# Performance work log

Measured on AMD Instinct MI355X. Metric: run time of the kernel, lower is better.

The kernel has to match this reference:

```python
import jax, jax.numpy as jnp
import numpy as np

EPS = 1e-8

def mlp(x, w1, b1, w2, b2):
    return jnp.tanh(x @ w1 + b1) @ w2 + b2

def setup_inputs() -> dict:
    key = jax.random.key(0)
    ks = jax.random.split(key, 24)
    N_NEWS, N_USERS, N_ATR = 50000, 100000, 1000
    E_ATR, E_USR = 100000, 2000000
    D = 768
    def lin(k, fi, fo):
        return jax.random.normal(k, (fi, fo), jnp.float32) * (1.0 / np.sqrt(fi))
    inp = {
        'news_x': jax.random.normal(ks[0], (N_NEWS, D), jnp.float32),
        'users_x': jax.random.normal(ks[1], (N_USERS, 128), jnp.float32),
        'w1a': lin(ks[2], D, 256), 'b1a': jnp.zeros((256,), jnp.float32),
        'w1b': lin(ks[3], 256, 128), 'b1b': jnp.zeros((128,), jnp.float32),
        'wna': lin(ks[4], D + 128, 512), 'bna': jnp.zeros((512,), jnp.float32),
        'wnb': lin(ks[5], 512, 128), 'bnb': jnp.zeros((128,), jnp.float32),
        'wua': lin(ks[6], 256, 256), 'bua': jnp.zeros((256,), jnp.float32),
        'wub': lin(ks[7], 256, 128), 'bub': jnp.zeros((128,), jnp.float32),
        'atr_row': jax.random.randint(ks[8], (E_ATR,), 0, N_NEWS, jnp.int32),
        'atr_col': jax.random.randint(ks[9], (E_ATR,), 0, N_ATR, jnp.int32),
        'usr_row': jax.random.randint(ks[10], (E_USR,), 0, N_NEWS, jnp.int32),
        'usr_col': jax.random.randint(ks[11], (E_USR,), 0, N_USERS, jnp.int32),
        'n_news': N_NEWS, 'n_users': N_USERS, 'n_atr': N_ATR,
    }
    return inp

def reference(news_x, users_x, w1a, b1a, w1b, b1b, wna, bna, wnb, bnb,
              wua, bua, wub, bub, atr_row, atr_col, usr_row, usr_col,
              n_news, n_users, n_atr):
    dt = news_x.dtype
    ones_a = jnp.ones(atr_row.shape[0], dt)
    ones_u = jnp.ones(usr_row.shape[0], dt)
    # FirstConv: news -> attribute nodes (edge_index.t() @ news)
    deg_atr = jax.ops.segment_sum(ones_a, atr_col, num_segments=n_atr)
    agr_atr = jax.ops.segment_sum(news_x[atr_row], atr_col, num_segments=n_atr)
    agr_atr = agr_atr / (deg_atr[:, None] + EPS)
    atr_feats = mlp(agr_atr, w1a, b1a, w1b, b1b)  # [n_atr, 128]
    # NewsConv: attribute -> news (edge_index @ atr_feats), concat with news_x
    deg_news = jax.ops.segment_sum(ones_a, atr_row, num_segments=n_news)
    agr_news = jax.ops.segment_sum(atr_feats[atr_col], atr_row, num_segments=n_news)
    agr_news = agr_news / (deg_news[:, None] + EPS)
    news_out = mlp(jnp.concatenate([news_x, agr_news], axis=1), wna, bna, wnb, bnb)  # [n_news,128]
    # UserConv: news -> users (edge_index['users'].t() @ news), concat with users_x
    deg_usr = jax.ops.segment_sum(ones_u, usr_col, num_segments=n_users)
    agr_usr = jax.ops.segment_sum(news_out[usr_row], usr_col, num_segments=n_users)
    agr_usr = agr_usr / (deg_usr[:, None] + EPS)
    users_out = mlp(jnp.concatenate([users_x, agr_usr], axis=1), wua, bua, wub, bub)  # [n_users,128]
    # stack final news + user embeddings into one array
    return jnp.concatenate([news_out, users_out], axis=0)  # [n_news+n_users, 128]
```

## Files before the change

kernel.cpp:

```cpp
#include <hip/hip_runtime.h>

#define N_NEWS 50000
#define N_USERS 100000
#define N_ATR 1000
#define E_ATR 100000
#define E_USR 2000000
#define EPSF 1e-8f

#define ACAP 192
#define NCAP 24
#define P_USR 250
#define UPP 400
#define ACAPP 9216
#define EBLK_A 4096

typedef short s16x8 __attribute__((ext_vector_type(8)));
typedef float f32x4 __attribute__((ext_vector_type(4)));

__device__ inline ushort f2bf(float f) {
    uint u = __float_as_uint(f);
    u += 0x7fffu + ((u >> 16) & 1u);
    return (ushort)(u >> 16);
}
__device__ inline float bflo(uint v) { return __uint_as_float(v << 16); }
__device__ inline float bfhi(uint v) { return __uint_as_float(v & 0xffff0000u); }
__device__ inline float fast_tanh(float x) {
    x = fminf(fmaxf(x, -15.0f), 15.0f);
    float e = __expf(2.0f * x);
    return (e - 1.0f) / (e + 1.0f);
}

struct TrJob { const float* src; ushort* dst; int R, C, blkEnd; };

struct PrepArgs {
    const int *atr_row, *atr_col, *usr_row, *usr_col;
    int *cnt_atr, *cnt_news, *arena_cnt;
    int *ids_atr, *ids_news;
    unsigned long long* arena;
    const float *news_x, *users_x;
    ushort *news_bf, *users_bf;
    int pa, fa, tr, n1, n2;
    TrJob j[6];
};

__global__ void prep_k(PrepArgs A) {
    __shared__ float tile[32][33];
    __shared__ int cloc[256], cscn[256], sexc[256], cbase[256];
    __shared__ ushort stageI[EBLK_A];
    int b = blockIdx.x;
    int t = threadIdx.x;
    if (b < A.pa) {
        cloc[t] = 0;
        __syncthreads();
        int base = b * EBLK_A;
        int endE = base + EBLK_A; if (endE > E_USR) endE = E_USR;
        int n = endE - base;
        for (int e = base + t; e < endE; e += 256)
            atomicAdd(&cloc[A.usr_col[e] / UPP], 1);
        __syncthreads();
        cscn[t] = cloc[t];
        __syncthreads();
        for (int off = 1; off < 256; off <<= 1) {
            int v = (t >= off) ? cscn[t - off] : 0;
            __syncthreads();
            cscn[t] += v;
            __syncthreads();
        }
        sexc[t] = cscn[t] - cloc[t];
        if (t < P_USR) cbase[t] = atomicAdd(&A.arena_cnt[t], cloc[t]);
        cloc[t] = 0;
        __syncthreads();
        for (int e = base + t; e < endE; e += 256) {
            int p = A.usr_col[e] / UPP;
            int off = atomicAdd(&cloc[p], 1);
            stageI[sexc[p] + off] = (ushort)(e - base);
        }
        __syncthreads();
        for (int i = t; i < n; i += 256) {
            int e = base + stageI[i];
            int c = A.usr_col[e];
            int r = A.usr_row[e];
            int p = c / UPP;
            int dst = cbase[p] + (i - sexc[p]);
            if (dst < ACAPP)
                A.arena[(size_t)p * ACAPP + dst] =
                    ((unsigned long long)(uint)c << 32) | (uint)r;
        }
        return;
    }
    b -= A.pa;
    if (b < A.fa) {
        int total = 2 * E_ATR;
        int per = (total + A.fa - 1) / A.fa;
        int base = b * per;
        int endE = base + per; if (endE > total) endE = total;
        for (int e = base + t; e < endE; e += 256) {
            if (e < E_ATR) {
                int c = A.atr_col[e];
                int slot = atomicAdd(&A.cnt_atr[c], 1);
                if (slot < ACAP) A.ids_atr[(size_t)c * ACAP + slot] = A.atr_row[e];
            } else {
                int e2 = e - E_ATR;
                int r = A.atr_row[e2];
                int slot = atomicAdd(&A.cnt_news[r], 1);
                if (slot < NCAP) A.ids_news[(size_t)r * NCAP + slot] = A.atr_col[e2];
            }
        }
        return;
    }
    b -= A.fa;
    if (b < A.tr) {
        int ji = 0;
        while (b >= A.j[ji].blkEnd) ++ji;
        const TrJob& J = A.j[ji];
        int lb = b - (ji ? A.j[ji - 1].blkEnd : 0);
        int ctiles = J.C / 32;
        int bc = (lb % ctiles) * 32, br = (lb / ctiles) * 32;
        int tx = t & 31, ty = t >> 5;
        for (int i = 0; i < 4; ++i)
            tile[ty + i * 8][tx] = J.src[(size_t)(br + ty + i * 8) * J.C + bc + tx];
        __syncthreads();
        for (int i = 0; i < 4; ++i)
            J.dst[(size_t)(bc + ty + i * 8) * J.R + br + tx] = f2bf(tile[tx][ty + i * 8]);
        return;
    }
    b -= A.tr;
    int i = b * 256 + t;
    const float* src; ushort* dst;
    if (i < A.n1) { src = A.news_x; dst = A.news_bf; }
    else          { i -= A.n1; if (i >= A.n2) return; src = A.users_x; dst = A.users_bf; }
    float4 a = ((const float4*)src)[i];
    uint2 v;
    v.x = (uint)f2bf(a.x) | ((uint)f2bf(a.y) << 16);
    v.y = (uint)f2bf(a.z) | ((uint)f2bf(a.w) << 16);
    ((uint2*)dst)[i] = v;
}

struct MidArgs {
    const unsigned long long* arena;
    const int* arena_cnt;
    int *cnt_usr, *start_usr, *ids_usr;
    const ushort* news_bf;
    const int* ids_atr;
    const int* cnt_atr;
    ushort* agr_atr_b;
};

__global__ void mid_k(MidArgs M) {
    __shared__ int cnt[512];
    __shared__ int scn[512];
    int b = blockIdx.x;
    int t = threadIdx.x;
    if (b < P_USR) {
        int p = b;
        int nA = M.arena_cnt[p]; if (nA > ACAPP) nA = ACAPP;
        const unsigned long long* ar = M.arena + (size_t)p * ACAPP;
        cnt[t] = 0; cnt[t + 256] = 0;
        __syncthreads();
        for (int i = t; i < nA; i += 256)
            atomicAdd(&cnt[(int)(ar[i] >> 32) - p * UPP], 1);
        __syncthreads();
        scn[t] = cnt[t]; scn[t + 256] = cnt[t + 256];
        __syncthreads();
        for (int off = 1; off < 512; off <<= 1) {
            int v0 = (t >= off) ? scn[t - off] : 0;
            int v1 = ((t + 256) >= off) ? scn[t + 256 - off] : 0;
            __syncthreads();
            scn[t] += v0; scn[t + 256] += v1;
            __syncthreads();
        }
        for (int i = t; i < UPP; i += 256) {
            int u = p * UPP + i;
            M.cnt_usr[u] = cnt[i];
            M.start_usr[u] = p * ACAPP + (scn[i] - cnt[i]);
        }
        __syncthreads();
        for (int i = t; i < UPP; i += 256) cnt[i] = scn[i] - cnt[i];
        __syncthreads();
        for (int i = t; i < nA; i += 256) {
            unsigned long long v = ar[i];
            int c = (int)(v >> 32);
            int off = atomicAdd(&cnt[c - p * UPP], 1);
            M.ids_usr[(size_t)p * ACAPP + off] = (int)(v & 0xffffffffu);
        }
        return;
    }
    b -= P_USR;
    int u = b;
    int dc = M.cnt_atr[u];
    int d = dc < ACAP ? dc : ACAP;
    const int* bp = M.ids_atr + (size_t)u * ACAP;
    const ushort* src = M.news_bf;
    float a0 = 0.f, a1 = 0.f, a2 = 0.f, a3 = 0.f;
    int i = 0;
    for (; i + 3 < d; i += 4) {
        const uint* r0 = (const uint*)(src + (size_t)bp[i] * 768);
        const uint* r1 = (const uint*)(src + (size_t)bp[i + 1] * 768);
        const uint* r2 = (const uint*)(src + (size_t)bp[i + 2] * 768);
        const uint* r3 = (const uint*)(src + (size_t)bp[i + 3] * 768);
        uint v0 = r0[t], v1 = r1[t], v2 = r2[t], v3 = r3[t];
        a0 += bflo(v0) + bflo(v1) + bflo(v2) + bflo(v3);
        a1 += bfhi(v0) + bfhi(v1) + bfhi(v2) + bfhi(v3);
        if (t < 128) {
            uint w0 = r0[t + 256], w1 = r1[t + 256], w2 = r2[t + 256], w3 = r3[t + 256];
            a2 += bflo(w0) + bflo(w1) + bflo(w2) + bflo(w3);
            a3 += bfhi(w0) + bfhi(w1) + bfhi(w2) + bfhi(w3);
        }
    }
    for (; i < d; ++i) {
        const uint* r0 = (const uint*)(src + (size_t)bp[i] * 768);
        uint v0 = r0[t];
        a0 += bflo(v0); a1 += bfhi(v0);
        if (t < 128) {
            uint v1 = r0[t + 256];
            a2 += bflo(v1); a3 += bfhi(v1);
        }
    }
    float inv = 1.0f / ((float)dc + EPSF);
    uint* dst = (uint*)(M.agr_atr_b + (size_t)u * 768);
    dst[t] = (uint)f2bf(a0 * inv) | ((uint)f2bf(a1 * inv) << 16);
    if (t < 128)
        dst[256 + t] = (uint)f2bf(a2 * inv) | ((uint)f2bf(a3 * inv) << 16);
}

template<int CAP>
__global__ void gather128c_k(const ushort* __restrict__ srcp, const int* __restrict__ ids,
                             const int* __restrict__ cnt, ushort* __restrict__ agr, int n) {
    int u = blockIdx.x * 8 + (threadIdx.x >> 5);
    if (u >= n) return;
    int lane = threadIdx.x & 31;
    int dc = cnt[u];
    int d = dc < CAP ? dc : CAP;
    const int* bp = ids + (size_t)u * CAP;
    float a0 = 0.f, a1 = 0.f, a2 = 0.f, a3 = 0.f;
    int i = 0;
    for (; i + 3 < d; i += 4) {
        int s0 = bp[i], s1 = bp[i + 1], s2 = bp[i + 2], s3 = bp[i + 3];
        uint2 v0 = *((const uint2*)(srcp + (size_t)s0 * 128) + lane);
        uint2 v1 = *((const uint2*)(srcp + (size_t)s1 * 128) + lane);
        uint2 v2 = *((const uint2*)(srcp + (size_t)s2 * 128) + lane);
        uint2 v3 = *((const uint2*)(srcp + (size_t)s3 * 128) + lane);
        a0 += bflo(v0.x) + bflo(v1.x) + bflo(v2.x) + bflo(v3.x);
        a1 += bfhi(v0.x) + bfhi(v1.x) + bfhi(v2.x) + bfhi(v3.x);
        a2 += bflo(v0.y) + bflo(v1.y) + bflo(v2.y) + bflo(v3.y);
        a3 += bfhi(v0.y) + bfhi(v1.y) + bfhi(v2.y) + bfhi(v3.y);
    }
    for (; i < d; ++i) {
        uint2 v0 = *((const uint2*)(srcp + (size_t)bp[i] * 128) + lane);
        a0 += bflo(v0.x); a1 += bfhi(v0.x);
        a2 += bflo(v0.y); a3 += bfhi(v0.y);
    }
    float inv = 1.0f / ((float)dc + EPSF);
    uint2 packed;
    packed.x = (uint)f2bf(a0 * inv) | ((uint)f2bf(a1 * inv) << 16);
    packed.y = (uint)f2bf(a2 * inv) | ((uint)f2bf(a3 * inv) << 16);
    *((uint2*)(agr + (size_t)u * 128) + lane) = packed;
}

__global__ void gather128s_k(const ushort* __restrict__ srcp, const int* __restrict__ ids,
                             const int* __restrict__ start, const int* __restrict__ cnt,
                             ushort* __restrict__ agr, int n) {
    int u = blockIdx.x * 8 + (threadIdx.x >> 5);
    if (u >= n) return;
    int lane = threadIdx.x & 31;
    int d = cnt[u];
    const int* bp = ids + start[u];
    float a0 = 0.f, a1 = 0.f, a2 = 0.f, a3 = 0.f;
    int i = 0;
    for (; i + 3 < d; i += 4) {
        int s0 = bp[i], s1 = bp[i + 1], s2 = bp[i + 2], s3 = bp[i + 3];
        uint2 v0 = *((const uint2*)(srcp + (size_t)s0 * 128) + lane);
        uint2 v1 = *((const uint2*)(srcp + (size_t)s1 * 128) + lane);
        uint2 v2 = *((const uint2*)(srcp + (size_t)s2 * 128) + lane);
        uint2 v3 = *((const uint2*)(srcp + (size_t)s3 * 128) + lane);
        a0 += bflo(v0.x) + bflo(v1.x) + bflo(v2.x) + bflo(v3.x);
        a1 += bfhi(v0.x) + bfhi(v1.x) + bfhi(v2.x) + bfhi(v3.x);
        a2 += bflo(v0.y) + bflo(v1.y) + bflo(v2.y) + bflo(v3.y);
        a3 += bfhi(v0.y) + bfhi(v1.y) + bfhi(v2.y) + bfhi(v3.y);
    }
    for (; i < d; ++i) {
        uint2 v0 = *((const uint2*)(srcp + (size_t)bp[i] * 128) + lane);
        a0 += bflo(v0.x); a1 += bfhi(v0.x);
        a2 += bflo(v0.y); a3 += bfhi(v0.y);
    }
    float inv = 1.0f / ((float)d + EPSF);
    uint2 packed;
    packed.x = (uint)f2bf(a0 * inv) | ((uint)f2bf(a1 * inv) << 16);
    packed.y = (uint)f2bf(a2 * inv) | ((uint)f2bf(a3 * inv) << 16);
    *((uint2*)(agr + (size_t)u * 128) + lane) = packed;
}

template<int NS, int NS1, bool TANH, int OMODE, int GY>
__launch_bounds__(256, 3)
__global__ void gemm5_k(const ushort* __restrict__ A1, const ushort* __restrict__ A2,
                        const ushort* __restrict__ Bt, const float* __restrict__ bias,
                        float* __restrict__ outf, ushort* __restrict__ outb,
                        int M, int N) {
    __shared__ __align__(16) char lds[32768];
    const int t = threadIdx.x;
    const int w = t >> 6, l = t & 63, lr = l & 15, lk = l >> 4;
    const int wm = w >> 1, wn = w & 1;
    int nwg = gridDim.x;
    int q = nwg >> 3, r = nwg & 7;
    int xcd = blockIdx.x & 7, idx = blockIdx.x >> 3;
    int fid = (xcd < r) ? xcd * (q + 1) + idx : r * (q + 1) + (xcd - r) * q + idx;
    constexpr int LG = (GY == 4) ? 2 : (GY == 2) ? 1 : 0;
    const int row0 = (fid >> LG) * 128;
    const int col0 = (fid & (GY - 1)) * 128;
    constexpr int A1RB = NS1 * 128;
    constexpr int A2RB = (NS - NS1) * 128;
    constexpr int BRB = NS * 128;

    auto stage = [&](int s) {
        const char* abase; int arb, soff;
        if (s < NS1) { abase = (const char*)A1; arb = A1RB; soff = s * 128; }
        else         { abase = (const char*)A2; arb = A2RB; soff = (s - NS1) * 128; }
#pragma unroll
        for (int i = 0; i < 4; ++i) {
            int chunk = i * 256 + w * 64 + l;
            int row = chunk >> 3, sub = chunk & 7;
            int rg = row0 + row; if (rg >= M) rg = M - 1;
            const char* src = abase + (size_t)rg * arb + soff + ((sub * 16) ^ ((row & 7) << 4));
            __builtin_amdgcn_global_load_lds(
                (const __attribute__((address_space(1))) unsigned int*)src,
                (__attribute__((address_space(3))) unsigned int*)(lds + i * 4096 + w * 1024),
                16, 0, 0);
        }
#pragma unroll
        for (int i = 0; i < 4; ++i) {
            int chunk = i * 256 + w * 64 + l;
            int row = chunk >> 3, sub = chunk & 7;
            const char* src = (const char*)Bt + (size_t)(col0 + row) * BRB + s * 128
                              + ((sub * 16) ^ ((row & 7) << 4));
            __builtin_amdgcn_global_load_lds(
                (const __attribute__((address_space(1))) unsigned int*)src,
                (__attribute__((address_space(3))) unsigned int*)(lds + 16384 + i * 4096 + w * 1024),
                16, 0, 0);
        }
    };

    f32x4 acc[4][4];
#pragma unroll
    for (int i = 0; i < 4; ++i)
#pragma unroll
        for (int j = 0; j < 4; ++j) acc[i][j] = (f32x4)0.f;

    stage(0);
    for (int s = 0; s < NS; ++s) {
        __syncthreads();
#pragma unroll
        for (int ks = 0; ks < 2; ++ks) {
            s16x8 af[4], bf[4];
#pragma unroll
            for (int rt = 0; rt < 4; ++rt) {
                int rr = wm * 64 + rt * 16 + lr;
                af[rt] = *(const s16x8*)(lds + rr * 128 + ((ks * 64 + lk * 16) ^ ((rr & 7) << 4)));
            }
#pragma unroll
            for (int ct = 0; ct < 4; ++ct) {
                int c = wn * 64 + ct * 16 + lr;
                bf[ct] = *(const s16x8*)(lds + 16384 + c * 128 + ((ks * 64 + lk * 16) ^ ((c & 7) << 4)));
            }
#pragma unroll
            for (int rt = 0; rt < 4; ++rt)
#pragma unroll
                for (int ct = 0; ct < 4; ++ct)
                    acc[rt][ct] = __builtin_amdgcn_mfma_f32_16x16x32_bf16(
                        af[rt], bf[ct], acc[rt][ct], 0, 0, 0);
        }
        __syncthreads();
        if (s + 1 < NS) stage(s + 1);
    }

    if (OMODE == 0) {
#pragma unroll
        for (int rt = 0; rt < 4; ++rt)
#pragma unroll
            for (int ct = 0; ct < 4; ++ct) {
                int c = wn * 64 + ct * 16 + lr;
                float bs = bias[col0 + c];
#pragma unroll
                for (int r4 = 0; r4 < 4; ++r4) {
                    int rr = wm * 64 + rt * 16 + lk * 4 + r4;
                    float v = acc[rt][ct][r4] + bs;
                    if (TANH) v = fast_tanh(v);
                    *(ushort*)(lds + rr * 256 + ((c * 2) ^ ((rr & 7) << 4))) = f2bf(v);
                }
            }
        __syncthreads();
#pragma unroll
        for (int i = 0; i < 8; ++i) {
            int chunk = i * 256 + t;
            int rr = chunk >> 4, cb = (chunk & 15) * 16;
            int rg = row0 + rr;
            if (rg < M)
                *(float4*)((char*)outb + (size_t)rg * (N * 2) + col0 * 2 + cb) =
                    *(const float4*)(lds + rr * 256 + (cb ^ ((rr & 7) << 4)));
        }
    } else {
#pragma unroll
        for (int rt = 0; rt < 4; ++rt)
#pragma unroll
            for (int ct = 0; ct < 4; ++ct) {
                int c = col0 + wn * 64 + ct * 16 + lr;
                float bs = bias[c];
#pragma unroll
                for (int r4 = 0; r4 < 4; ++r4) {
                    int rg = row0 + wm * 64 + rt * 16 + lk * 4 + r4;
                    if (rg < M) {
                        float v = acc[rt][ct][r4] + bs;
                        if (TANH) v = fast_tanh(v);
                        outf[(size_t)rg * N + c] = v;
                        if (OMODE == 2) outb[(size_t)rg * N + c] = f2bf(v);
                    }
                }
            }
    }
}

__launch_bounds__(256, 3)
__global__ void mlp_users_fused(const ushort* __restrict__ users_bf,
                                const ushort* __restrict__ agr_b,
                                const ushort* __restrict__ wuat,
                                const float* __restrict__ bua,
                                const ushort* __restrict__ wubt,
                                const float* __restrict__ bub,
                                float* __restrict__ outf, int M) {
    __shared__ __align__(16) char lds[32768];
    const int t = threadIdx.x;
    const int w = t >> 6, l = t & 63, lr = l & 15, lk = l >> 4;
    const int row0 = blockIdx.x * 64;

#pragma unroll
    for (int i = 0; i < 8; ++i) {
        int chunk = i * 256 + w * 64 + l;
        int row = chunk >> 5;
        int rg = row0 + row; if (rg >= M) rg = M - 1;
        int off = ((chunk * 16) & 511) ^ ((row & 7) << 4);
        int sc = off >> 4;
        const char* src = (sc < 16)
            ? (const char*)users_bf + (size_t)rg * 256 + sc * 16
            : (const char*)agr_b + (size_t)rg * 256 + (sc - 16) * 16;
        __builtin_amdgcn_global_load_lds(
            (const __attribute__((address_space(1))) unsigned int*)src,
            (__attribute__((address_space(3))) unsigned int*)(lds + i * 4096 + w * 1024),
            16, 0, 0);
    }
    __syncthreads();

    f32x4 acc[4][4];
#pragma unroll
    for (int i = 0; i < 4; ++i)
#pragma unroll
        for (int j = 0; j < 4; ++j) acc[i][j] = (f32x4)0.f;
#pragma unroll
    for (int ks = 0; ks < 8; ++ks) {
        s16x8 af[4], bf[4];
#pragma unroll
        for (int rt = 0; rt < 4; ++rt) {
            int rr = rt * 16 + lr;
            af[rt] = *(const s16x8*)(lds + ((rr * 512 + ks * 64 + lk * 16) ^ ((rr & 7) << 4)));
        }
#pragma unroll
        for (int ct = 0; ct < 4; ++ct) {
            int c = w * 64 + ct * 16 + lr;
            bf[ct] = *(const s16x8*)(wuat + (size_t)c * 256 + ks * 32 + lk * 8);
        }
#pragma unroll
        for (int rt = 0; rt < 4; ++rt)
#pragma unroll
            for (int ct = 0; ct < 4; ++ct)
                acc[rt][ct] = __builtin_amdgcn_mfma_f32_16x16x32_bf16(
                    af[rt], bf[ct], acc[rt][ct], 0, 0, 0);
    }
    __syncthreads();

#pragma unroll
    for (int rt = 0; rt < 4; ++rt)
#pragma unroll
        for (int ct = 0; ct < 4; ++ct) {
            int c = w * 64 + ct * 16 + lr;
            float bs = bua[c];
#pragma unroll
            for (int r4 = 0; r4 < 4; ++r4) {
                int rr = rt * 16 + lk * 4 + r4;
                ushort h = f2bf(fast_tanh(acc[rt][ct][r4] + bs));
                *(ushort*)(lds + ((rr * 512 + c * 2) ^ ((rr & 7) << 4))) = h;
            }
        }
    __syncthreads();

    f32x4 acc2[4][2];
#pragma unroll
    for (int i = 0; i < 4; ++i)
#pragma unroll
        for (int j = 0; j < 2; ++j) acc2[i][j] = (f32x4)0.f;
#pragma unroll
    for (int ks = 0; ks < 8; ++ks) {
        s16x8 af[4], bf[2];
#pragma unroll
        for (int rt = 0; rt < 4; ++rt) {
            int rr = rt * 16 + lr;
            af[rt] = *(const s16x8*)(lds + ((rr * 512 + ks * 64 + lk * 16) ^ ((rr & 7) << 4)));
        }
#pragma unroll
        for (int ct = 0; ct < 2; ++ct) {
            int c = w * 32 + ct * 16 + lr;
            bf[ct] = *(const s16x8*)(wubt + (size_t)c * 256 + ks * 32 + lk * 8);
        }
#pragma unroll
        for (int rt = 0; rt < 4; ++rt)
#pragma unroll
            for (int ct = 0; ct < 2; ++ct)
                acc2[rt][ct] = __builtin_amdgcn_mfma_f32_16x16x32_bf16(
                    af[rt], bf[ct], acc2[rt][ct], 0, 0, 0);
    }
#pragma unroll
    for (int rt = 0; rt < 4; ++rt)
#pragma unroll
        for (int ct = 0; ct < 2; ++ct) {
            int c = w * 32 + ct * 16 + lr;
            float bs = bub[c];
#pragma unroll
            for (int r4 = 0; r4 < 4; ++r4) {
                int rg = row0 + rt * 16 + lk * 4 + r4;
                if (rg < M) outf[(size_t)rg * 128 + c] = acc2[rt][ct][r4] + bs;
            }
        }
}

extern "C" void kernel_launch(void* const* d_in, const int* in_sizes, int n_in,
                              void* d_out, int out_size, void* d_ws, size_t ws_size,
                              hipStream_t stream) {
    const float* news_x  = (const float*)d_in[0];
    const float* users_x = (const float*)d_in[1];
    const float* w1a = (const float*)d_in[2];
    const float* b1a = (const float*)d_in[3];
    const float* w1b = (const float*)d_in[4];
    const float* b1b = (const float*)d_in[5];
    const float* wna = (const float*)d_in[6];
    const float* bna = (const float*)d_in[7];
    const float* wnb = (const float*)d_in[8];
    const float* bnb = (const float*)d_in[9];
    const float* wua = (const float*)d_in[10];
    const float* bua = (const float*)d_in[11];
    const float* wub = (const float*)d_in[12];
    const float* bub = (const float*)d_in[13];
    const int* atr_row = (const int*)d_in[14];
    const int* atr_col = (const int*)d_in[15];
    const int* usr_row = (const int*)d_in[16];
    const int* usr_col = (const int*)d_in[17];

    char* ws = (char*)d_ws;
    size_t o = 0;
    auto alloc = [&](size_t bytes) { void* p = ws + o; o += (bytes + 255) & ~(size_t)255; return p; };

    int* cnt_atr   = (int*)alloc(N_ATR * 4);
    int* cnt_news  = (int*)alloc(N_NEWS * 4);
    int* arena_cnt = (int*)alloc(P_USR * 4);
    size_t zero_bytes = o;
    int* cnt_usr   = (int*)alloc((size_t)N_USERS * 4);
    int* start_usr = (int*)alloc((size_t)N_USERS * 4);
    int* ids_atr  = (int*)alloc((size_t)N_ATR * ACAP * 4);
    int* ids_news = (int*)alloc((size_t)N_NEWS * NCAP * 4);
    int* ids_usr  = (int*)alloc((size_t)P_USR * ACAPP * 4);
    unsigned long long* arena = (unsigned long long*)alloc((size_t)P_USR * ACAPP * 8);
    ushort* news_bf    = (ushort*)alloc((size_t)N_NEWS * 768 * 2);
    ushort* users_bf   = (ushort*)alloc((size_t)N_USERS * 128 * 2);
    ushort* agr_atr_b  = (ushort*)alloc((size_t)N_ATR * 768 * 2);
    ushort* h_atr_b    = (ushort*)alloc((size_t)N_ATR * 256 * 2);
    ushort* atr_feats_b= (ushort*)alloc((size_t)N_ATR * 128 * 2);
    ushort* agr_news_b = (ushort*)alloc((size_t)N_NEWS * 128 * 2);
    ushort* agr_usr_b  = (ushort*)alloc((size_t)N_USERS * 128 * 2);
    ushort* out_news_b = (ushort*)alloc((size_t)N_NEWS * 128 * 2);
    ushort* h_buf      = (ushort*)alloc((size_t)N_NEWS * 512 * 2);
    ushort* w1at = (ushort*)alloc((size_t)256 * 768 * 2);
    ushort* w1bt = (ushort*)alloc((size_t)128 * 256 * 2);
    ushort* wnat = (ushort*)alloc((size_t)512 * 896 * 2);
    ushort* wnbt = (ushort*)alloc((size_t)128 * 512 * 2);
    ushort* wuat = (ushort*)alloc((size_t)256 * 256 * 2);
    ushort* wubt = (ushort*)alloc((size_t)128 * 256 * 2);

    float* out = (float*)d_out;
    float* out_users = out + (size_t)N_NEWS * 128;

    hipMemsetAsync(cnt_atr, 0, zero_bytes, stream);

    {
        PrepArgs A;
        A.atr_row = atr_row; A.atr_col = atr_col;
        A.usr_row = usr_row; A.usr_col = usr_col;
        A.cnt_atr = cnt_atr; A.cnt_news = cnt_news; A.arena_cnt = arena_cnt;
        A.ids_atr = ids_atr; A.ids_news = ids_news;
        A.arena = arena;
        A.news_x = news_x; A.users_x = users_x;
        A.news_bf = news_bf; A.users_bf = users_bf;
        A.pa = (E_USR + EBLK_A - 1) / EBLK_A;
        A.fa = 25;
        A.n1 = N_NEWS * 768 / 4;
        A.n2 = N_USERS * 128 / 4;
        int acc2 = 0;
        auto add = [&](int i, const float* s, ushort* d, int R, int C) {
            acc2 += (C / 32) * (R / 32);
            A.j[i] = TrJob{s, d, R, C, acc2};
        };
        add(0, w1a, w1at, 768, 256);
        add(1, w1b, w1bt, 256, 128);
        add(2, wna, wnat, 896, 512);
        add(3, wnb, wnbt, 512, 128);
        add(4, wua, wuat, 256, 256);
        add(5, wub, wubt, 256, 128);
        A.tr = acc2;
        int cvt_blk = (A.n1 + A.n2 + 255) / 256;
        prep_k<<<A.pa + A.fa + A.tr + cvt_blk, 256, 0, stream>>>(A);
    }

    {
        MidArgs M;
        M.arena = arena; M.arena_cnt = arena_cnt;
        M.cnt_usr = cnt_usr; M.start_usr = start_usr; M.ids_usr = ids_usr;
        M.news_bf = news_bf; M.ids_atr = ids_atr; M.cnt_atr = cnt_atr;
        M.agr_atr_b = agr_atr_b;
        mid_k<<<P_USR + N_ATR, 256, 0, stream>>>(M);
    }

    gemm5_k<12, 12, true, 0, 2><<<16, 256, 0, stream>>>(
        agr_atr_b, nullptr, w1at, b1a, nullptr, h_atr_b, N_ATR, 256);
    gemm5_k<4, 4, false, 0, 1><<<8, 256, 0, stream>>>(
        h_atr_b, nullptr, w1bt, b1b, nullptr, atr_feats_b, N_ATR, 128);
    gather128c_k<NCAP><<<(N_NEWS + 7) / 8, 256, 0, stream>>>(
        atr_feats_b, ids_news, cnt_news, agr_news_b, N_NEWS);

    gemm5_k<14, 12, true, 0, 4><<<391 * 4, 256, 0, stream>>>(
        news_bf, agr_news_b, wnat, bna, nullptr, h_buf, N_NEWS, 512);
    gemm5_k<8, 8, false, 2, 1><<<391, 256, 0, stream>>>(
        h_buf, nullptr, wnbt, bnb, out, out_news_b, N_NEWS, 128);

    gather128s_k<<<(N_USERS + 7) / 8, 256, 0, stream>>>(
        out_news_b, ids_usr, start_usr, cnt_usr, agr_usr_b, N_USERS);
    mlp_users_fused<<<(N_USERS + 63) / 64, 256, 0, stream>>>(
        users_bf, agr_usr_b, wuat, bua, wubt, bub, out_users, N_USERS);
}
```

Baseline: 407.7 us.

## Fuse fp32-to-bf16 input conversion into consumer kernels, drop the conversion pass

Removes the separate pass in prep_k that converted news_x and users_x to bf16 buffers. The attribute gather in mid_k now reads fp32 rows directly, and the news GEMM and user MLP convert fp32 to bf16 while staging tiles into LDS through registers instead of async global_load_lds. This avoids writing and re-reading about 90 MB of bf16 copies. In exchange it reads fp32 (twice the bytes) inside the GEMM loads, and the news GEMM loses asynchronous direct-to-LDS loading for its first operand, which can hurt latency hiding. Because news_x is staged across 4 column blocks, each row is now read and converted four times in fp32.

```diff
diff --git a/kernel.cpp b/kernel.cpp
--- a/kernel.cpp
+++ b/kernel.cpp
@@ -29,6 +29,16 @@
     float e = __expf(2.0f * x);
     return (e - 1.0f) / (e + 1.0f);
 }
+__device__ inline s16x8 cvt8(const float* p) {
+    float4 x0 = *(const float4*)p;
+    float4 x1 = *(const float4*)(p + 4);
+    s16x8 v;
+    v[0] = (short)f2bf(x0.x); v[1] = (short)f2bf(x0.y);
+    v[2] = (short)f2bf(x0.z); v[3] = (short)f2bf(x0.w);
+    v[4] = (short)f2bf(x1.x); v[5] = (short)f2bf(x1.y);
+    v[6] = (short)f2bf(x1.z); v[7] = (short)f2bf(x1.w);
+    return v;
+}
 
 struct TrJob { const float* src; ushort* dst; int R, C, blkEnd; };
 
@@ -37,9 +47,7 @@
     int *cnt_atr, *cnt_news, *arena_cnt;
     int *ids_atr, *ids_news;
     unsigned long long* arena;
-    const float *news_x, *users_x;
-    ushort *news_bf, *users_bf;
-    int pa, fa, tr, n1, n2;
+    int pa, fa, tr;
     TrJob j[6];
 };
 
@@ -109,38 +117,25 @@
         return;
     }
     b -= A.fa;
-    if (b < A.tr) {
-        int ji = 0;
-        while (b >= A.j[ji].blkEnd) ++ji;
-        const TrJob& J = A.j[ji];
-        int lb = b - (ji ? A.j[ji - 1].blkEnd : 0);
-        int ctiles = J.C / 32;
-        int bc = (lb % ctiles) * 32, br = (lb / ctiles) * 32;
-        int tx = t & 31, ty = t >> 5;
-        for (int i = 0; i < 4; ++i)
-            tile[ty + i * 8][tx] = J.src[(size_t)(br + ty + i * 8) * J.C + bc + tx];
-        __syncthreads();
-        for (int i = 0; i < 4; ++i)
-            J.dst[(size_t)(bc + ty + i * 8) * J.R + br + tx] = f2bf(tile[tx][ty + i * 8]);
-        return;
-    }
-    b -= A.tr;
-    int i = b * 256 + t;
-    const float* src; ushort* dst;
-    if (i < A.n1) { src = A.news_x; dst = A.news_bf; }
-    else          { i -= A.n1; if (i >= A.n2) return; src = A.users_x; dst = A.users_bf; }
-    float4 a = ((const float4*)src)[i];
-    uint2 v;
-    v.x = (uint)f2bf(a.x) | ((uint)f2bf(a.y) << 16);
-    v.y = (uint)f2bf(a.z) | ((uint)f2bf(a.w) << 16);
-    ((uint2*)dst)[i] = v;
+    int ji = 0;
+    while (b >= A.j[ji].blkEnd) ++ji;
+    const TrJob& J = A.j[ji];
+    int lb = b - (ji ? A.j[ji - 1].blkEnd : 0);
+    int ctiles = J.C / 32;
+    int bc = (lb % ctiles) * 32, br = (lb / ctiles) * 32;
+    int tx = t & 31, ty = t >> 5;
+    for (int i = 0; i < 4; ++i)
+        tile[ty + i * 8][tx] = J.src[(size_t)(br + ty + i * 8) * J.C + bc + tx];
+    __syncthreads();
+    for (int i = 0; i < 4; ++i)
+        J.dst[(size_t)(bc + ty + i * 8) * J.R + br + tx] = f2bf(tile[tx][ty + i * 8]);
 }
 
 struct MidArgs {
     const unsigned long long* arena;
     const int* arena_cnt;
     int *cnt_usr, *start_usr, *ids_usr;
-    const ushort* news_bf;
+    const float* news_x;
     const int* ids_atr;
     const int* cnt_atr;
     ushort* agr_atr_b;
@@ -190,30 +185,29 @@
     int dc = M.cnt_atr[u];
     int d = dc < ACAP ? dc : ACAP;
     const int* bp = M.ids_atr + (size_t)u * ACAP;
-    const ushort* src = M.news_bf;
     float a0 = 0.f, a1 = 0.f, a2 = 0.f, a3 = 0.f;
     int i = 0;
     for (; i + 3 < d; i += 4) {
-        const uint* r0 = (const uint*)(src + (size_t)bp[i] * 768);
-        const uint* r1 = (const uint*)(src + (size_t)bp[i + 1] * 768);
-        const uint* r2 = (const uint*)(src + (size_t)bp[i + 2] * 768);
-        const uint* r3 = (const uint*)(src + (size_t)bp[i + 3] * 768);
-        uint v0 = r0[t], v1 = r1[t], v2 = r2[t], v3 = r3[t];
-        a0 += bflo(v0) + bflo(v1) + bflo(v2) + bflo(v3);
-        a1 += bfhi(v0) + bfhi(v1) + bfhi(v2) + bfhi(v3);
+        const float2* r0 = (const float2*)(M.news_x + (size_t)bp[i] * 768);
+        const float2* r1 = (const float2*)(M.news_x + (size_t)bp[i + 1] * 768);
+        const float2* r2 = (const float2*)(M.news_x + (size_t)bp[i + 2] * 768);
+        const float2* r3 = (const float2*)(M.news_x + (size_t)bp[i + 3] * 768);
+        float2 v0 = r0[t], v1 = r1[t], v2 = r2[t], v3 = r3[t];
+        a0 += v0.x + v1.x + v2.x + v3.x;
+        a1 += v0.y + v1.y + v2.y + v3.y;
         if (t < 128) {
-            uint w0 = r0[t + 256], w1 = r1[t + 256], w2 = r2[t + 256], w3 = r3[t + 256];
-            a2 += bflo(w0) + bflo(w1) + bflo(w2) + bflo(w3);
-            a3 += bfhi(w0) + bfhi(w1) + bfhi(w2) + bfhi(w3);
+            float2 w0 = r0[256 + t], w1 = r1[256 + t], w2 = r2[256 + t], w3 = r3[256 + t];
+            a2 += w0.x + w1.x + w2.x + w3.x;
+            a3 += w0.y + w1.y + w2.y + w3.y;
         }
     }
     for (; i < d; ++i) {
-        const uint* r0 = (const uint*)(src + (size_t)bp[i] * 768);
-        uint v0 = r0[t];
-        a0 += bflo(v0); a1 += bfhi(v0);
+        const float2* r0 = (const float2*)(M.news_x + (size_t)bp[i] * 768);
+        float2 v0 = r0[t];
+        a0 += v0.x; a1 += v0.y;
         if (t < 128) {
-            uint v1 = r0[t + 256];
-            a2 += bflo(v1); a3 += bfhi(v1);
+            float2 w0 = r0[256 + t];
+            a2 += w0.x; a3 += w0.y;
         }
     }
     float inv = 1.0f / ((float)dc + EPSF);
@@ -290,7 +284,7 @@
     *((uint2*)(agr + (size_t)u * 128) + lane) = packed;
 }
 
-template<int NS, int NS1, bool TANH, int OMODE, int GY>
+template<int NS, int NS1, bool TANH, int OMODE, int GY, bool A1F32>
 __launch_bounds__(256, 3)
 __global__ void gemm5_k(const ushort* __restrict__ A1, const ushort* __restrict__ A2,
                         const ushort* __restrict__ Bt, const float* __restrict__ bias,
@@ -312,19 +306,31 @@
     constexpr int BRB = NS * 128;
 
     auto stage = [&](int s) {
-        const char* abase; int arb, soff;
-        if (s < NS1) { abase = (const char*)A1; arb = A1RB; soff = s * 128; }
-        else         { abase = (const char*)A2; arb = A2RB; soff = (s - NS1) * 128; }
-#pragma unroll
-        for (int i = 0; i < 4; ++i) {
-            int chunk = i * 256 + w * 64 + l;
-            int row = chunk >> 3, sub = chunk & 7;
-            int rg = row0 + row; if (rg >= M) rg = M - 1;
-            const char* src = abase + (size_t)rg * arb + soff + ((sub * 16) ^ ((row & 7) << 4));
-            __builtin_amdgcn_global_load_lds(
-                (const __attribute__((address_space(1))) unsigned int*)src,
-                (__attribute__((address_space(3))) unsigned int*)(lds + i * 4096 + w * 1024),
-                16, 0, 0);
+        if (A1F32 && s < NS1) {
+            const float* Af = (const float*)A1;
+#pragma unroll
+            for (int i = 0; i < 4; ++i) {
+                int chunk = i * 256 + t;
+                int row = chunk >> 3, sub = chunk & 7;
+                int rg = row0 + row; if (rg >= M) rg = M - 1;
+                s16x8 v = cvt8(Af + (size_t)rg * (NS1 * 64) + s * 64 + sub * 8);
+                *(s16x8*)(lds + row * 128 + ((sub * 16) ^ ((row & 7) << 4))) = v;
+            }
+        } else {
+            const char* abase; int arb, soff;
+            if (s < NS1) { abase = (const char*)A1; arb = A1RB; soff = s * 128; }
+            else         { abase = (const char*)A2; arb = A2RB; soff = (s - NS1) * 128; }
+#pragma unroll
+            for (int i = 0; i < 4; ++i) {
+                int chunk = i * 256 + w * 64 + l;
+                int row = chunk >> 3, sub = chunk & 7;
+                int rg = row0 + row; if (rg >= M) rg = M - 1;
+                const char* src = abase + (size_t)rg * arb + soff + ((sub * 16) ^ ((row & 7) << 4));
+                __builtin_amdgcn_global_load_lds(
+                    (const __attribute__((address_space(1))) unsigned int*)src,
+                    (__attribute__((address_space(3))) unsigned int*)(lds + i * 4096 + w * 1024),
+                    16, 0, 0);
+            }
         }
 #pragma unroll
         for (int i = 0; i < 4; ++i) {
@@ -419,7 +425,7 @@
 }
 
 __launch_bounds__(256, 3)
-__global__ void mlp_users_fused(const ushort* __restrict__ users_bf,
+__global__ void mlp_users_fused(const float* __restrict__ users_x,
                                 const ushort* __restrict__ agr_b,
                                 const ushort* __restrict__ wuat,
                                 const float* __restrict__ bua,
@@ -433,18 +439,13 @@
 
 #pragma unroll
     for (int i = 0; i < 8; ++i) {
-        int chunk = i * 256 + w * 64 + l;
-        int row = chunk >> 5;
+        int chunk = i * 256 + t;
+        int row = chunk >> 5, sc = chunk & 31;
         int rg = row0 + row; if (rg >= M) rg = M - 1;
-        int off = ((chunk * 16) & 511) ^ ((row & 7) << 4);
-        int sc = off >> 4;
-        const char* src = (sc < 16)
-            ? (const char*)users_bf + (size_t)rg * 256 + sc * 16
-            : (const char*)agr_b + (size_t)rg * 256 + (sc - 16) * 16;
-        __builtin_amdgcn_global_load_lds(
-            (const __attribute__((address_space(1))) unsigned int*)src,
-            (__attribute__((address_space(3))) unsigned int*)(lds + i * 4096 + w * 1024),
-            16, 0, 0);
+        s16x8 v;
+        if (sc < 16) v = cvt8(users_x + (size_t)rg * 128 + sc * 8);
+        else         v = *(const s16x8*)(agr_b + (size_t)rg * 128 + (sc - 16) * 8);
+        *(s16x8*)(lds + ((row * 512 + sc * 16) ^ ((row & 7) << 4))) = v;
     }
     __syncthreads();
 
@@ -565,8 +566,6 @@
     int* ids_news = (int*)alloc((size_t)N_NEWS * NCAP * 4);
     int* ids_usr  = (int*)alloc((size_t)P_USR * ACAPP * 4);
     unsigned long long* arena = (unsigned long long*)alloc((size_t)P_USR * ACAPP * 8);
-    ushort* news_bf    = (ushort*)alloc((size_t)N_NEWS * 768 * 2);
-    ushort* users_bf   = (ushort*)alloc((size_t)N_USERS * 128 * 2);
     ushort* agr_atr_b  = (ushort*)alloc((size_t)N_ATR * 768 * 2);
     ushort* h_atr_b    = (ushort*)alloc((size_t)N_ATR * 256 * 2);
     ushort* atr_feats_b= (ushort*)alloc((size_t)N_ATR * 128 * 2);
@@ -593,12 +592,8 @@
         A.cnt_atr = cnt_atr; A.cnt_news = cnt_news; A.arena_cnt = arena_cnt;
         A.ids_atr = ids_atr; A.ids_news = ids_news;
         A.arena = arena;
-        A.news_x = news_x; A.users_x = users_x;
-        A.news_bf = news_bf; A.users_bf = users_bf;
         A.pa = (E_USR + EBLK_A - 1) / EBLK_A;
         A.fa = 25;
-        A.n1 = N_NEWS * 768 / 4;
-        A.n2 = N_USERS * 128 / 4;
         int acc2 = 0;
         auto add = [&](int i, const float* s, ushort* d, int R, int C) {
             acc2 += (C / 32) * (R / 32);
@@ -611,33 +606,32 @@
         add(4, wua, wuat, 256, 256);
         add(5, wub, wubt, 256, 128);
         A.tr = acc2;
-        int cvt_blk = (A.n1 + A.n2 + 255) / 256;
-        prep_k<<<A.pa + A.fa + A.tr + cvt_blk, 256, 0, stream>>>(A);
+        prep_k<<<A.pa + A.fa + A.tr, 256, 0, stream>>>(A);
     }
 
     {
         MidArgs M;
         M.arena = arena; M.arena_cnt = arena_cnt;
         M.cnt_usr = cnt_usr; M.start_usr = start_usr; M.ids_usr = ids_usr;
-        M.news_bf = news_bf; M.ids_atr = ids_atr; M.cnt_atr = cnt_atr;
+        M.news_x = news_x; M.ids_atr = ids_atr; M.cnt_atr = cnt_atr;
         M.agr_atr_b = agr_atr_b;
         mid_k<<<P_USR + N_ATR, 256, 0, stream>>>(M);
     }
 
-    gemm5_k<12, 12, true, 0, 2><<<16, 256, 0, stream>>>(
+    gemm5_k<12, 12, true, 0, 2, false><<<16, 256, 0, stream>>>(
         agr_atr_b, nullptr, w1at, b1a, nullptr, h_atr_b, N_ATR, 256);
-    gemm5_k<4, 4, false, 0, 1><<<8, 256, 0, stream>>>(
+    gemm5_k<4, 4, false, 0, 1, false><<<8, 256, 0, stream>>>(
         h_atr_b, nullptr, w1bt, b1b, nullptr, atr_feats_b, N_ATR, 128);
     gather128c_k<NCAP><<<(N_NEWS + 7) / 8, 256, 0, stream>>>(
         atr_feats_b, ids_news, cnt_news, agr_news_b, N_NEWS);
 
-    gemm5_k<14, 12, true, 0, 4><<<391 * 4, 256, 0, stream>>>(
-        news_bf, agr_news_b, wnat, bna, nullptr, h_buf, N_NEWS, 512);
-    gemm5_k<8, 8, false, 2, 1><<<391, 256, 0, stream>>>(
+    gemm5_k<14, 12, true, 0, 4, true><<<391 * 4, 256, 0, stream>>>(
+        (const ushort*)news_x, agr_news_b, wnat, bna, nullptr, h_buf, N_NEWS, 512);
+    gemm5_k<8, 8, false, 2, 1, false><<<391, 256, 0, stream>>>(
         h_buf, nullptr, wnbt, bnb, out, out_news_b, N_NEWS, 128);
 
     gather128s_k<<<(N_USERS + 7) / 8, 256, 0, stream>>>(
         out_news_b, ids_usr, start_usr, cnt_usr, agr_usr_b, N_USERS);
     mlp_users_fused<<<(N_USERS + 63) / 64, 256, 0, stream>>>(
-        users_bf, agr_usr_b, wuat, bua, wubt, bub, out_users, N_USERS);
-}
+        users_x, agr_usr_b, wuat, bua, wubt, bub, out_users, N_USERS);
+}
```

Result: slower. 460.8 us (+13.0%).
